# Performance work log

Hardware: AMD Instinct MI355X
Metric: run time of the kernel (lower is better)

Reference implementation:

```python
import jax, jax.numpy as jnp
import numpy as np

# --- config (matches init_kwargs) ---
B, L = 16, 1024            # batch, max_seq_len
S = L - 1                  # effective sequence length
D = 768                    # attention_dim
H = 8                      # n_heads
DH = D // 3 * 2            # per-head Q/K/V out dim = 512
HID = 256                  # hidden_dim (EntireEmbedding output)
FF = 3072                  # ffnn_dim
N_A = 10000                # n_assessments = offsets[0]
N_CATE, N_CONT = 4, 6
EPS = 1e-5


def setup_inputs() -> dict:
    key = jax.random.key(0)
    ks = jax.random.split(key, 24)
    f = lambda k, shp, s=0.02: (jax.random.normal(k, shp, dtype=jnp.float32) * s)
    inp = {
        "cate_x": jax.random.randint(ks[0], (B, L, N_CATE), 0, N_A),
        "cont_x": jax.random.normal(ks[1], (B, L, N_CONT), dtype=jnp.float32),
        "mask": jax.random.randint(ks[2], (B, L), 0, 2),
        "targets": jax.random.randint(ks[3], (B, L), 0, 2),
        # embeddings (padding_idx=0 rows zeroed)
        "M_emb": f(ks[4], ((N_A + 1) * 2 - 1, D)).at[0].set(0.0),
        "E_emb": f(ks[5], (N_A + 1, D)).at[0].set(0.0),
        "pos_emb": f(ks[6], (S, D)),
        # EntireEmbedding stand-in: cate embedding + linear over cont feats -> HID
        "cate_emb": f(ks[7], (N_A + 1, HID)).at[0].set(0.0),
        "cont_W": f(ks[8], (N_CONT, HID)),
        "cont_b": jnp.zeros((HID,), jnp.float32),
        # per-head Q/K/V, stacked over head axis
        "WQ": f(ks[9], (H, D, DH)),
        "bQ": jnp.zeros((H, DH), jnp.float32),
        "WK": f(ks[10], (H, D + HID, DH)),
        "bK": jnp.zeros((H, DH), jnp.float32),
        "WV": f(ks[11], (H, D + HID, DH)),
        "bV": jnp.zeros((H, DH), jnp.float32),
        "W0": f(ks[12], (H * DH, D)),
        "ln_g": jnp.ones((D,), jnp.float32),
        "ln_b": jnp.zeros((D,), jnp.float32),
        "ffn_W1": f(ks[13], (D, FF)),
        "ffn_b1": jnp.zeros((FF,), jnp.float32),
        "ffn_W2": f(ks[14], (FF, D)),
        "ffn_b2": jnp.zeros((D,), jnp.float32),
        # FinalConnecting stand-in: Linear(D, 1)
        "fin_W": f(ks[15], (D, 1)),
        "fin_b": jnp.zeros((1,), jnp.float32),
    }
    return inp


def reference(cate_x, cont_x, mask, targets, M_emb, E_emb, pos_emb, cate_emb,
              cont_W, cont_b, WQ, bQ, WK, bK, WV, bV, W0, ln_g, ln_b,
              ffn_W1, ffn_b1, ffn_W2, ffn_b2, fin_W, fin_b):
    # additive mask, faithful to the original (triu over [B,S]!)
    new_mask = jnp.triu(jnp.ones((B, S), jnp.float32), k=-1) * 100000.0 - 100000.0

    assessments = cate_x[:, :-1, 0]                 # [B,S]
    interactions = targets[:, :-1]
    y = assessments + interactions * N_A            # interaction ids
    next_assessments = cate_x[:, 1:, 0]

    M_hat = M_emb[y] + pos_emb[None]                # [B,S,D]
    comb = cate_emb[cate_x[..., 0]] + cont_x @ cont_W + cont_b   # [B,L,HID]
    E_hat = jnp.concatenate([E_emb[next_assessments], comb[:, 1:, :]], axis=-1)  # [B,S,D+HID]

    # all heads at once (faithful per-head Q/K/V linears, stacked)
    Q = jnp.einsum('bsd,hde->hbse', M_hat, WQ) + bQ[:, None, None, :]
    K = jnp.einsum('bsd,hde->hbse', E_hat, WK) + bK[:, None, None, :]
    V = jnp.einsum('bsd,hde->hbse', E_hat, WV) + bV[:, None, None, :]

    score = jnp.einsum('hbqe,hbke->hbqk', Q, K) / jnp.sqrt(jnp.asarray(DH, Q.dtype))
    score = score + new_mask[None, :, None, :]      # broadcast over query axis
    attn = jax.nn.softmax(score, axis=-1)
    Z = jnp.einsum('hbqk,hbke->hbqe', attn, V)      # [H,B,S,DH]
    Zc = jnp.transpose(Z, (1, 2, 0, 3)).reshape(B, S, H * DH)  # head-major concat

    z = Zc @ W0                                     # [B,S,D]
    fz = jax.nn.relu(z @ ffn_W1 + ffn_b1) @ ffn_W2 + ffn_b2  # dropout off (eval)
    h = z + fz
    mu = jnp.mean(h, axis=-1, keepdims=True)
    var = jnp.mean((h - mu) ** 2, axis=-1, keepdims=True)
    zn = (h - mu) / jnp.sqrt(var + EPS) * ln_g + ln_b

    out = (zn @ fin_W + fin_b)[..., 0]              # [B,S]
    return out
```

## Files before the change

kernel.cpp:

```cpp
#include <hip/hip_runtime.h>
#include <hip/hip_bf16.h>

constexpr int B_   = 16;
constexpr int L_   = 1024;
constexpr int S_   = 1023;
constexpr int D_   = 768;
constexpr int H_   = 8;
constexpr int DH_  = 512;
constexpr int HID_ = 256;
constexpr int FF_  = 3072;
constexpr int NA_  = 10000;
constexpr int NCATE_ = 4;
constexpr int NCONT_ = 6;
constexpr float EPS_ = 1e-5f;
constexpr long BSR_ = (long)B_ * S_;
constexpr int SLD_ = 1024;

constexpr long COMB_SZ = BSR_ * HID_;
constexpr long IDX_PAD = 49152;
constexpr long QKV_SZ  = BSR_ * DH_;
constexpr long SC_SZ   = (long)B_ * S_ * SLD_;
constexpr long ZO_SZ   = BSR_ * D_;
constexpr size_t WS_NEED_BYTES =
    (size_t)(COMB_SZ + IDX_PAD + 3 * QKV_SZ + SC_SZ + ZO_SZ) * 4;

__device__ __forceinline__ float blk_reduce_sum(float v, float* sm) {
#pragma unroll
    for (int off = 32; off > 0; off >>= 1) v += __shfl_down(v, off, 64);
    const int lane = threadIdx.x & 63, wv = threadIdx.x >> 6;
    if (lane == 0) sm[wv] = v;
    __syncthreads();
    float t = (threadIdx.x < 4) ? sm[threadIdx.x] : 0.f;
    t += __shfl_down(t, 2, 64);
    t += __shfl_down(t, 1, 64);
    if (threadIdx.x == 0) sm[4] = t;
    __syncthreads();
    float r = sm[4];
    __syncthreads();
    return r;
}

__device__ __forceinline__ float blk_reduce_max(float v, float* sm) {
#pragma unroll
    for (int off = 32; off > 0; off >>= 1) v = fmaxf(v, __shfl_down(v, off, 64));
    const int lane = threadIdx.x & 63, wv = threadIdx.x >> 6;
    if (lane == 0) sm[wv] = v;
    __syncthreads();
    float t = (threadIdx.x < 4) ? sm[threadIdx.x] : -3.4e38f;
    t = fmaxf(t, __shfl_down(t, 2, 64));
    t = fmaxf(t, __shfl_down(t, 1, 64));
    if (threadIdx.x == 0) sm[4] = t;
    __syncthreads();
    float r = sm[4];
    __syncthreads();
    return r;
}

__global__ __launch_bounds__(256) void sentinel_k(float* __restrict__ out, int n)
{
    const int i = blockIdx.x * 256 + threadIdx.x;
    if (i < n) out[i] = 1e30f;
}

__global__ __launch_bounds__(256) void prep_k(
    const int* __restrict__ cate_x, const float* __restrict__ cont_x,
    const int* __restrict__ targets,
    const float* __restrict__ cate_emb, const float* __restrict__ cont_W,
    const float* __restrict__ cont_b,
    int* __restrict__ yArr, int* __restrict__ nxArr, int* __restrict__ sArr,
    float* __restrict__ comb)
{
    const int row = blockIdx.x;
    const int b = row / S_;
    const int s = row - b * S_;
    const int nx = cate_x[((long)b * L_ + s + 1) * NCATE_];
    if (threadIdx.x == 0) {
        yArr[row]  = cate_x[((long)b * L_ + s) * NCATE_] + targets[(long)b * L_ + s] * NA_;
        nxArr[row] = nx;
        sArr[row]  = s;
    }
    const float* cx = cont_x + ((long)b * L_ + s + 1) * NCONT_;
    float cv[NCONT_];
#pragma unroll
    for (int i = 0; i < NCONT_; ++i) cv[i] = cx[i];
    const int j = threadIdx.x;
    float acc = cont_b[j];
#pragma unroll
    for (int i = 0; i < NCONT_; ++i) acc = fmaf(cv[i], cont_W[i * HID_ + j], acc);
    comb[(long)row * HID_ + j] = cate_emb[(long)nx * HID_ + j] + acc;
}

template<int AMODE, bool TB, bool BIAS, bool RELU, bool ADDC, bool ACCUM>
__global__ __launch_bounds__(256) void sgemm_k(
    const float* __restrict__ A, const float* __restrict__ A2,
    const int* __restrict__ rIdx, const int* __restrict__ rS,
    const float* __restrict__ Bm,
    const float* __restrict__ bias, const float* __restrict__ Cadd,
    float* __restrict__ C,
    int M, int N, int Kd, int lda, int ldb, int ldc,
    long sA, long sB, long sC, float alpha)
{
    constexpr int BM = 128, BN = 128, BK = 16;
    __shared__ float As[BK][BM];
    __shared__ float Bs[BK][BN];

    const int tid = threadIdx.x;
    const int tx = tid & 15;
    const int ty = tid >> 4;
    const int rowBase = blockIdx.y * BM;
    const int colBase = blockIdx.x * BN;
    const int bz = blockIdx.z;
    if constexpr (AMODE == 0) A += (long)bz * sA;
    Bm += (long)bz * sB;
    C += (long)bz * sC;
    if constexpr (ADDC) Cadd += (long)bz * sC;

    float acc[8][8];
#pragma unroll
    for (int i = 0; i < 8; ++i)
#pragma unroll
        for (int j = 0; j < 8; ++j) acc[i][j] = 0.f;

    for (int k0 = 0; k0 < Kd; k0 += BK) {
#pragma unroll
        for (int u = 0; u < 2; ++u) {
            const int f = tid + u * 256;
            const int r = f >> 2;
            const int k4 = (f & 3) * 4;
            const int gk = k0 + k4;
            float v0 = 0.f, v1 = 0.f, v2 = 0.f, v3 = 0.f;
            const int gr = rowBase + r;
            if (gr < M) {
                if constexpr (AMODE == 0) {
                    const float* p = A + (long)gr * lda + gk;
                    if (gk + 3 < Kd) {
                        float4 v = *(const float4*)p;
                        v0 = v.x; v1 = v.y; v2 = v.z; v3 = v.w;
                    } else {
                        if (gk + 0 < Kd) v0 = p[0];
                        if (gk + 1 < Kd) v1 = p[1];
                        if (gk + 2 < Kd) v2 = p[2];
                        if (gk + 3 < Kd) v3 = p[3];
                    }
                } else if constexpr (AMODE == 1) {
                    const int y = rIdx[gr];
                    const int s = rS[gr];
                    const float4 a = *(const float4*)(A  + (long)y * D_ + gk);
                    const float4 p = *(const float4*)(A2 + (long)s * D_ + gk);
                    v0 = a.x + p.x; v1 = a.y + p.y; v2 = a.z + p.z; v3 = a.w + p.w;
                } else {
                    if (gk < D_) {
                        const int nx = rIdx[gr];
                        const float4 a = *(const float4*)(A + (long)nx * D_ + gk);
                        v0 = a.x; v1 = a.y; v2 = a.z; v3 = a.w;
                    } else {
                        const float4 a = *(const float4*)(A2 + (long)gr * HID_ + (gk - D_));
                        v0 = a.x; v1 = a.y; v2 = a.z; v3 = a.w;
                    }
                }
            }
            As[k4 + 0][r] = v0; As[k4 + 1][r] = v1;
            As[k4 + 2][r] = v2; As[k4 + 3][r] = v3;
        }
        if constexpr (!TB) {
#pragma unroll
            for (int u = 0; u < 2; ++u) {
                const int f = tid + u * 256;
                const int kk = f >> 5;
                const int n4 = (f & 31) * 4;
                float v0 = 0.f, v1 = 0.f, v2 = 0.f, v3 = 0.f;
                const int gk = k0 + kk;
                const int gc = colBase + n4;
                if (gk < Kd) {
                    const float* p = Bm + (long)gk * ldb + gc;
                    if (gc + 3 < N) {
                        float4 v = *(const float4*)p;
                        v0 = v.x; v1 = v.y; v2 = v.z; v3 = v.w;
                    } else {
                        if (gc + 0 < N) v0 = p[0];
                        if (gc + 1 < N) v1 = p[1];
                        if (gc + 2 < N) v2 = p[2];
                        if (gc + 3 < N) v3 = p[3];
                    }
                }
                Bs[kk][n4 + 0] = v0; Bs[kk][n4 + 1] = v1;
                Bs[kk][n4 + 2] = v2; Bs[kk][n4 + 3] = v3;
            }
        } else {
#pragma unroll
            for (int u = 0; u < 2; ++u) {
                const int f = tid + u * 256;
                const int n = f >> 2;
                const int k4 = (f & 3) * 4;
                float v0 = 0.f, v1 = 0.f, v2 = 0.f, v3 = 0.f;
                const int gn = colBase + n;
                if (gn < N) {
                    const float* p = Bm + (long)gn * ldb + k0 + k4;
                    if (k0 + k4 + 3 < Kd) {
                        float4 v = *(const float4*)p;
                        v0 = v.x; v1 = v.y; v2 = v.z; v3 = v.w;
                    } else {
                        if (k0 + k4 + 0 < Kd) v0 = p[0];
                        if (k0 + k4 + 1 < Kd) v1 = p[1];
                        if (k0 + k4 + 2 < Kd) v2 = p[2];
                        if (k0 + k4 + 3 < Kd) v3 = p[3];
                    }
                }
                Bs[k4 + 0][n] = v0; Bs[k4 + 1][n] = v1;
                Bs[k4 + 2][n] = v2; Bs[k4 + 3][n] = v3;
            }
        }
        __syncthreads();

#pragma unroll
        for (int kk = 0; kk < BK; ++kk) {
            float a[8], b[8];
            *(float4*)&a[0] = *(const float4*)&As[kk][ty * 8];
            *(float4*)&a[4] = *(const float4*)&As[kk][ty * 8 + 4];
            *(float4*)&b[0] = *(const float4*)&Bs[kk][tx * 8];
            *(float4*)&b[4] = *(const float4*)&Bs[kk][tx * 8 + 4];
#pragma unroll
            for (int i = 0; i < 8; ++i)
#pragma unroll
                for (int j = 0; j < 8; ++j)
                    acc[i][j] = fmaf(a[i], b[j], acc[i][j]);
        }
        __syncthreads();
    }

#pragma unroll
    for (int i = 0; i < 8; ++i) {
        const int r = rowBase + ty * 8 + i;
        if (r >= M) continue;
#pragma unroll
        for (int j = 0; j < 8; ++j) {
            const int c = colBase + tx * 8 + j;
            if (c >= N) continue;
            float v = acc[i][j] * alpha;
            if constexpr (BIAS) v += bias[c];
            if constexpr (ADDC) v += Cadd[(long)r * ldc + c];
            if constexpr (RELU) v = fmaxf(v, 0.f);
            const long idx = (long)r * ldc + c;
            if constexpr (ACCUM) C[idx] += v; else C[idx] = v;
        }
    }
}

__global__ __launch_bounds__(256) void softmax_k(float* __restrict__ Sc)
{
    const int row = blockIdx.x;
    const int b = row / S_;
    float* s = Sc + (long)row * SLD_;
    __shared__ float buf[S_];
    __shared__ float sm[5];
    const int klo = b - 1;

    float m = -3.4e38f;
    for (int k = threadIdx.x; k < S_; k += 256) {
        float v = s[k];
        if (k < klo) v -= 1e5f;
        buf[k] = v;
        m = fmaxf(m, v);
    }
    m = blk_reduce_max(m, sm);
    float sum = 0.f;
    for (int k = threadIdx.x; k < S_; k += 256) {
        const float e = __expf(buf[k] - m);
        buf[k] = e;
        sum += e;
    }
    sum = blk_reduce_sum(sum, sm);
    const float inv = 1.0f / sum;
    for (int k = threadIdx.x; k < S_; k += 256) s[k] = buf[k] * inv;
}

__global__ __launch_bounds__(256) void final_k(
    const float* __restrict__ h, const float* __restrict__ g,
    const float* __restrict__ bt, const float* __restrict__ fw,
    const float* __restrict__ fb, float* __restrict__ out)
{
    const int row = blockIdx.x;
    const float* hr = h + (long)row * D_;
    __shared__ float sm[5];

    float lsum = 0.f;
    for (int d = threadIdx.x; d < D_; d += 256) lsum += hr[d];
    const float mu = blk_reduce_sum(lsum, sm) * (1.0f / D_);

    float lvar = 0.f;
    for (int d = threadIdx.x; d < D_; d += 256) {
        const float t = hr[d] - mu;
        lvar = fmaf(t, t, lvar);
    }
    const float var = blk_reduce_sum(lvar, sm) * (1.0f / D_);
    const float rstd = 1.0f / sqrtf(var + EPS_);

    float ldot = 0.f;
    for (int d = threadIdx.x; d < D_; d += 256) {
        const float zn = (hr[d] - mu) * rstd * g[d] + bt[d];
        ldot = fmaf(zn, fw[d], ldot);
    }
    const float dot = blk_reduce_sum(ldot, sm);
    if (threadIdx.x == 0) out[row] = dot + fb[0];
}

static inline dim3 gemm_grid(int M, int N, int batch) {
    return dim3((N + 127) / 128, (M + 127) / 128, batch);
}

extern "C" void kernel_launch(void* const* d_in, const int* in_sizes, int n_in,
                              void* d_out, int out_size, void* d_ws, size_t ws_size,
                              hipStream_t stream)
{
    float* out = (float*)d_out;

    if (ws_size < WS_NEED_BYTES) {
        sentinel_k<<<(out_size + 255) / 256, 256, 0, stream>>>(out, out_size);
        return;
    }

    const int*   cate_x   = (const int*)  d_in[0];
    const float* cont_x   = (const float*)d_in[1];
    const int*   targets  = (const int*)  d_in[3];
    const float* M_emb    = (const float*)d_in[4];
    const float* E_emb    = (const float*)d_in[5];
    const float* pos_emb  = (const float*)d_in[6];
    const float* cate_emb = (const float*)d_in[7];
    const float* cont_W   = (const float*)d_in[8];
    const float* cont_b   = (const float*)d_in[9];
    const float* WQ = (const float*)d_in[10];
    const float* bQ = (const float*)d_in[11];
    const float* WK = (const float*)d_in[12];
    const float* bK = (const float*)d_in[13];
    const float* WV = (const float*)d_in[14];
    const float* bV = (const float*)d_in[15];
    const float* W0 = (const float*)d_in[16];
    const float* ln_g = (const float*)d_in[17];
    const float* ln_b = (const float*)d_in[18];
    const float* W1 = (const float*)d_in[19];
    const float* b1 = (const float*)d_in[20];
    const float* W2 = (const float*)d_in[21];
    const float* b2 = (const float*)d_in[22];
    const float* fw = (const float*)d_in[23];
    const float* fb = (const float*)d_in[24];
    float* ws  = (float*)d_ws;

    float* comb  = ws;
    int*   yArr  = (int*)(ws + COMB_SZ);
    int*   nxArr = yArr + BSR_;
    int*   sArr  = nxArr + BSR_;
    float* Qh = ws + COMB_SZ + IDX_PAD;
    float* Kh = Qh + QKV_SZ;
    float* Vh = Kh + QKV_SZ;
    float* Sc = Vh + QKV_SZ;
    float* Zo = Sc + SC_SZ;
    float* Zh   = Qh;
    float* Hid  = Qh;
    float* Hbuf = Sc;

    prep_k<<<(int)BSR_, 256, 0, stream>>>(cate_x, cont_x, targets, cate_emb,
                                          cont_W, cont_b, yArr, nxArr, sArr, comb);

    const float inv_sqrt_dh = 0.044194173824159216f;

    for (int h = 0; h < H_; ++h) {
        sgemm_k<1, false, true, false, false, false><<<gemm_grid((int)BSR_, DH_, 1), 256, 0, stream>>>(
            M_emb, pos_emb, yArr, sArr,
            WQ + (long)h * D_ * DH_, bQ + (long)h * DH_, nullptr, Qh,
            (int)BSR_, DH_, D_, D_, DH_, DH_, 0, 0, 0, 1.0f);
        sgemm_k<2, false, true, false, false, false><<<gemm_grid((int)BSR_, DH_, 1), 256, 0, stream>>>(
            E_emb, comb, nxArr, nullptr,
            WK + (long)h * (D_ + HID_) * DH_, bK + (long)h * DH_, nullptr, Kh,
            (int)BSR_, DH_, D_ + HID_, 0, DH_, DH_, 0, 0, 0, 1.0f);
        sgemm_k<2, false, true, false, false, false><<<gemm_grid((int)BSR_, DH_, 1), 256, 0, stream>>>(
            E_emb, comb, nxArr, nullptr,
            WV + (long)h * (D_ + HID_) * DH_, bV + (long)h * DH_, nullptr, Vh,
            (int)BSR_, DH_, D_ + HID_, 0, DH_, DH_, 0, 0, 0, 1.0f);
        sgemm_k<0, true, false, false, false, false><<<gemm_grid(S_, S_, B_), 256, 0, stream>>>(
            Qh, nullptr, nullptr, nullptr,
            Kh, nullptr, nullptr, Sc,
            S_, S_, DH_, DH_, DH_, SLD_,
            (long)S_ * DH_, (long)S_ * DH_, (long)S_ * SLD_, inv_sqrt_dh);
        softmax_k<<<(int)BSR_, 256, 0, stream>>>(Sc);
        sgemm_k<0, false, false, false, false, false><<<gemm_grid(S_, DH_, B_), 256, 0, stream>>>(
            Sc, nullptr, nullptr, nullptr,
            Vh, nullptr, nullptr, Zh,
            S_, DH_, S_, SLD_, DH_, DH_,
            (long)S_ * SLD_, (long)S_ * DH_, (long)S_ * DH_, 1.0f);
        if (h == 0)
            sgemm_k<0, false, false, false, false, false><<<gemm_grid((int)BSR_, D_, 1), 256, 0, stream>>>(
                Zh, nullptr, nullptr, nullptr,
                W0 + (long)h * DH_ * D_, nullptr, nullptr, Zo,
                (int)BSR_, D_, DH_, DH_, D_, D_, 0, 0, 0, 1.0f);
        else
            sgemm_k<0, false, false, false, false, true><<<gemm_grid((int)BSR_, D_, 1), 256, 0, stream>>>(
                Zh, nullptr, nullptr, nullptr,
                W0 + (long)h * DH_ * D_, nullptr, nullptr, Zo,
                (int)BSR_, D_, DH_, DH_, D_, D_, 0, 0, 0, 1.0f);
    }

    for (int c = 0; c < 4; ++c) {
        const int f0 = c * 768;
        sgemm_k<0, false, true, true, false, false><<<gemm_grid((int)BSR_, 768, 1), 256, 0, stream>>>(
            Zo, nullptr, nullptr, nullptr,
            W1 + f0, b1 + f0, nullptr, Hid,
            (int)BSR_, 768, D_, D_, FF_, 768, 0, 0, 0, 1.0f);
        if (c == 0)
            sgemm_k<0, false, true, false, true, false><<<gemm_grid((int)BSR_, D_, 1), 256, 0, stream>>>(
                Hid, nullptr, nullptr, nullptr,
                W2 + (long)f0 * D_, b2, Zo, Hbuf,
                (int)BSR_, D_, 768, 768, D_, D_, 0, 0, 0, 1.0f);
        else
            sgemm_k<0, false, false, false, false, true><<<gemm_grid((int)BSR_, D_, 1), 256, 0, stream>>>(
                Hid, nullptr, nullptr, nullptr,
                W2 + (long)f0 * D_, nullptr, nullptr, Hbuf,
                (int)BSR_, D_, 768, 768, D_, D_, 0, 0, 0, 1.0f);
    }

    final_k<<<(int)BSR_, 256, 0, stream>>>(Hbuf, ln_g, ln_b, fw, fb, out);

    (void)in_sizes; (void)n_in;
}
```

Before: 13.02 ms.

## Parametrize SGEMM tile size, fuse K/V projections, and interleave thread tile mapping

Makes the SGEMM tile size a template parameter, using 64x64 tiles with 4x4 per-thread micro-tiles for most GEMMs and keeping 128x128 tiles for the QK^T score GEMM. The K and V projections now run in a single launch, with column blocks past DH routed to the V weights, bias and output. Each thread's elements are now strided by 64 in shared memory and the output, instead of sitting in one contiguous block of 8. The aim is more blocks in flight on the mid-size GEMMs and fewer launches and LDS conflicts. The cost is lower arithmetic intensity per thread with 4x4 micro-tiles.

```diff
diff --git a/kernel.cpp b/kernel.cpp
--- a/kernel.cpp
+++ b/kernel.cpp
@@ -90,40 +90,53 @@
     comb[(long)row * HID_ + j] = cate_emb[(long)nx * HID_ + j] + acc;
 }
 
-template<int AMODE, bool TB, bool BIAS, bool RELU, bool ADDC, bool ACCUM>
+template<int TSZ, int AMODE, bool TB, bool BIAS, bool RELU, bool ADDC, bool ACCUM, bool KVF>
 __global__ __launch_bounds__(256) void sgemm_k(
     const float* __restrict__ A, const float* __restrict__ A2,
     const int* __restrict__ rIdx, const int* __restrict__ rS,
-    const float* __restrict__ Bm,
-    const float* __restrict__ bias, const float* __restrict__ Cadd,
-    float* __restrict__ C,
+    const float* __restrict__ Bm, const float* __restrict__ Bm2,
+    const float* __restrict__ bias, const float* __restrict__ bias2,
+    const float* __restrict__ Cadd, float* __restrict__ C, float* __restrict__ C2,
     int M, int N, int Kd, int lda, int ldb, int ldc,
     long sA, long sB, long sC, float alpha)
 {
-    constexpr int BM = 128, BN = 128, BK = 16;
-    __shared__ float As[BK][BM];
-    __shared__ float Bs[BK][BN];
+    constexpr int BK = 16;
+    constexpr int TM = TSZ / 16;
+    constexpr int NL = TSZ / 64;
+    constexpr int NF4M = TSZ / 4 - 1;
+    constexpr int SHB  = (TSZ == 128) ? 5 : 4;
+    __shared__ float As[BK][TSZ];
+    __shared__ float Bs[BK][TSZ];
 
     const int tid = threadIdx.x;
     const int tx = tid & 15;
     const int ty = tid >> 4;
-    const int rowBase = blockIdx.y * BM;
-    const int colBase = blockIdx.x * BN;
+    const int rowBase = blockIdx.y * TSZ;
+    int colBase = blockIdx.x * TSZ;
     const int bz = blockIdx.z;
+
+    if constexpr (KVF) {
+        if (colBase >= DH_) {
+            Bm = Bm2;
+            if constexpr (BIAS) bias = bias2;
+            C = C2;
+            colBase -= DH_;
+        }
+    }
     if constexpr (AMODE == 0) A += (long)bz * sA;
     Bm += (long)bz * sB;
     C += (long)bz * sC;
     if constexpr (ADDC) Cadd += (long)bz * sC;
 
-    float acc[8][8];
-#pragma unroll
-    for (int i = 0; i < 8; ++i)
-#pragma unroll
-        for (int j = 0; j < 8; ++j) acc[i][j] = 0.f;
+    float acc[TM][TM];
+#pragma unroll
+    for (int i = 0; i < TM; ++i)
+#pragma unroll
+        for (int j = 0; j < TM; ++j) acc[i][j] = 0.f;
 
     for (int k0 = 0; k0 < Kd; k0 += BK) {
 #pragma unroll
-        for (int u = 0; u < 2; ++u) {
+        for (int u = 0; u < NL; ++u) {
             const int f = tid + u * 256;
             const int r = f >> 2;
             const int k4 = (f & 3) * 4;
@@ -140,7 +153,6 @@
                         if (gk + 0 < Kd) v0 = p[0];
                         if (gk + 1 < Kd) v1 = p[1];
                         if (gk + 2 < Kd) v2 = p[2];
-                        if (gk + 3 < Kd) v3 = p[3];
                     }
                 } else if constexpr (AMODE == 1) {
                     const int y = rIdx[gr];
@@ -164,13 +176,13 @@
         }
         if constexpr (!TB) {
 #pragma unroll
-            for (int u = 0; u < 2; ++u) {
+            for (int u = 0; u < NL; ++u) {
                 const int f = tid + u * 256;
-                const int kk = f >> 5;
-                const int n4 = (f & 31) * 4;
-                float v0 = 0.f, v1 = 0.f, v2 = 0.f, v3 = 0.f;
+                const int kk = f >> SHB;
+                const int n4 = (f & NF4M) * 4;
                 const int gk = k0 + kk;
                 const int gc = colBase + n4;
+                float v0 = 0.f, v1 = 0.f, v2 = 0.f, v3 = 0.f;
                 if (gk < Kd) {
                     const float* p = Bm + (long)gk * ldb + gc;
                     if (gc + 3 < N) {
@@ -188,7 +200,7 @@
             }
         } else {
 #pragma unroll
-            for (int u = 0; u < 2; ++u) {
+            for (int u = 0; u < NL; ++u) {
                 const int f = tid + u * 256;
                 const int n = f >> 2;
                 const int k4 = (f & 3) * 4;
@@ -214,27 +226,28 @@
 
 #pragma unroll
         for (int kk = 0; kk < BK; ++kk) {
-            float a[8], b[8];
-            *(float4*)&a[0] = *(const float4*)&As[kk][ty * 8];
-            *(float4*)&a[4] = *(const float4*)&As[kk][ty * 8 + 4];
-            *(float4*)&b[0] = *(const float4*)&Bs[kk][tx * 8];
-            *(float4*)&b[4] = *(const float4*)&Bs[kk][tx * 8 + 4];
-#pragma unroll
-            for (int i = 0; i < 8; ++i)
-#pragma unroll
-                for (int j = 0; j < 8; ++j)
+            float a[TM], b[TM];
+#pragma unroll
+            for (int ih = 0; ih < TM / 4; ++ih) {
+                *(float4*)&a[ih * 4] = *(const float4*)&As[kk][ih * 64 + ty * 4];
+                *(float4*)&b[ih * 4] = *(const float4*)&Bs[kk][ih * 64 + tx * 4];
+            }
+#pragma unroll
+            for (int i = 0; i < TM; ++i)
+#pragma unroll
+                for (int j = 0; j < TM; ++j)
                     acc[i][j] = fmaf(a[i], b[j], acc[i][j]);
         }
         __syncthreads();
     }
 
 #pragma unroll
-    for (int i = 0; i < 8; ++i) {
-        const int r = rowBase + ty * 8 + i;
+    for (int i = 0; i < TM; ++i) {
+        const int r = rowBase + (i >> 2) * 64 + ty * 4 + (i & 3);
         if (r >= M) continue;
 #pragma unroll
-        for (int j = 0; j < 8; ++j) {
-            const int c = colBase + tx * 8 + j;
+        for (int j = 0; j < TM; ++j) {
+            const int c = colBase + (j >> 2) * 64 + tx * 4 + (j & 3);
             if (c >= N) continue;
             float v = acc[i][j] * alpha;
             if constexpr (BIAS) v += bias[c];
@@ -304,8 +317,8 @@
     if (threadIdx.x == 0) out[row] = dot + fb[0];
 }
 
-static inline dim3 gemm_grid(int M, int N, int batch) {
-    return dim3((N + 127) / 128, (M + 127) / 128, batch);
+static inline dim3 ggrid(int M, int N, int batch, int tsz) {
+    return dim3((N + tsz - 1) / tsz, (M + tsz - 1) / tsz, batch);
 }
 
 extern "C" void kernel_launch(void* const* d_in, const int* in_sizes, int n_in,
@@ -313,7 +326,6 @@
                               hipStream_t stream)
 {
     float* out = (float*)d_out;
-
     if (ws_size < WS_NEED_BYTES) {
         sentinel_k<<<(out_size + 255) / 256, 256, 0, stream>>>(out, out_size);
         return;
@@ -364,56 +376,71 @@
     const float inv_sqrt_dh = 0.044194173824159216f;
 
     for (int h = 0; h < H_; ++h) {
-        sgemm_k<1, false, true, false, false, false><<<gemm_grid((int)BSR_, DH_, 1), 256, 0, stream>>>(
+        sgemm_k<64, 1, false, true, false, false, false, false>
+            <<<ggrid((int)BSR_, DH_, 1, 64), 256, 0, stream>>>(
             M_emb, pos_emb, yArr, sArr,
-            WQ + (long)h * D_ * DH_, bQ + (long)h * DH_, nullptr, Qh,
+            WQ + (long)h * D_ * DH_, nullptr, bQ + (long)h * DH_, nullptr,
+            nullptr, Qh, nullptr,
             (int)BSR_, DH_, D_, D_, DH_, DH_, 0, 0, 0, 1.0f);
-        sgemm_k<2, false, true, false, false, false><<<gemm_grid((int)BSR_, DH_, 1), 256, 0, stream>>>(
+        sgemm_k<64, 2, false, true, false, false, false, true>
+            <<<ggrid((int)BSR_, 2 * DH_, 1, 64), 256, 0, stream>>>(
             E_emb, comb, nxArr, nullptr,
-            WK + (long)h * (D_ + HID_) * DH_, bK + (long)h * DH_, nullptr, Kh,
-            (int)BSR_, DH_, D_ + HID_, 0, DH_, DH_, 0, 0, 0, 1.0f);
-        sgemm_k<2, false, true, false, false, false><<<gemm_grid((int)BSR_, DH_, 1), 256, 0, stream>>>(
-            E_emb, comb, nxArr, nullptr,
-            WV + (long)h * (D_ + HID_) * DH_, bV + (long)h * DH_, nullptr, Vh,
-            (int)BSR_, DH_, D_ + HID_, 0, DH_, DH_, 0, 0, 0, 1.0f);
-        sgemm_k<0, true, false, false, false, false><<<gemm_grid(S_, S_, B_), 256, 0, stream>>>(
+            WK + (long)h * (D_ + HID_) * DH_, WV + (long)h * (D_ + HID_) * DH_,
+            bK + (long)h * DH_, bV + (long)h * DH_,
+            nullptr, Kh, Vh,
+            (int)BSR_, 2 * DH_, D_ + HID_, 0, DH_, DH_, 0, 0, 0, 1.0f);
+        sgemm_k<128, 0, true, false, false, false, false, false>
+            <<<ggrid(S_, S_, B_, 128), 256, 0, stream>>>(
             Qh, nullptr, nullptr, nullptr,
-            Kh, nullptr, nullptr, Sc,
+            Kh, nullptr, nullptr, nullptr,
+            nullptr, Sc, nullptr,
             S_, S_, DH_, DH_, DH_, SLD_,
             (long)S_ * DH_, (long)S_ * DH_, (long)S_ * SLD_, inv_sqrt_dh);
         softmax_k<<<(int)BSR_, 256, 0, stream>>>(Sc);
-        sgemm_k<0, false, false, false, false, false><<<gemm_grid(S_, DH_, B_), 256, 0, stream>>>(
+        sgemm_k<64, 0, false, false, false, false, false, false>
+            <<<ggrid(S_, DH_, B_, 64), 256, 0, stream>>>(
             Sc, nullptr, nullptr, nullptr,
-            Vh, nullptr, nullptr, Zh,
+            Vh, nullptr, nullptr, nullptr,
+            nullptr, Zh, nullptr,
             S_, DH_, S_, SLD_, DH_, DH_,
             (long)S_ * SLD_, (long)S_ * DH_, (long)S_ * DH_, 1.0f);
         if (h == 0)
-            sgemm_k<0, false, false, false, false, false><<<gemm_grid((int)BSR_, D_, 1), 256, 0, stream>>>(
+            sgemm_k<64, 0, false, false, false, false, false, false>
+                <<<ggrid((int)BSR_, D_, 1, 64), 256, 0, stream>>>(
                 Zh, nullptr, nullptr, nullptr,
-                W0 + (long)h * DH_ * D_, nullptr, nullptr, Zo,
+                W0 + (long)h * DH_ * D_, nullptr, nullptr, nullptr,
+                nullptr, Zo, nullptr,
                 (int)BSR_, D_, DH_, DH_, D_, D_, 0, 0, 0, 1.0f);
         else
-            sgemm_k<0, false, false, false, false, true><<<gemm_grid((int)BSR_, D_, 1), 256, 0, stream>>>(
+            sgemm_k<64, 0, false, false, false, false, true, false>
+                <<<ggrid((int)BSR_, D_, 1, 64), 256, 0, stream>>>(
                 Zh, nullptr, nullptr, nullptr,
-                W0 + (long)h * DH_ * D_, nullptr, nullptr, Zo,
+                W0 + (long)h * DH_ * D_, nullptr, nullptr, nullptr,
+                nullptr, Zo, nullptr,
                 (int)BSR_, D_, DH_, DH_, D_, D_, 0, 0, 0, 1.0f);
     }
 
     for (int c = 0; c < 4; ++c) {
         const int f0 = c * 768;
-        sgemm_k<0, false, true, true, false, false><<<gemm_grid((int)BSR_, 768, 1), 256, 0, stream>>>(
+        sgemm_k<64, 0, false, true, true, false, false, false>
+            <<<ggrid((int)BSR_, 768, 1, 64), 256, 0, stream>>>(
             Zo, nullptr, nullptr, nullptr,
-            W1 + f0, b1 + f0, nullptr, Hid,
+            W1 + f0, nullptr, b1 + f0, nullptr,
+            nullptr, Hid, nullptr,
             (int)BSR_, 768, D_, D_, FF_, 768, 0, 0, 0, 1.0f);
         if (c == 0)
-            sgemm_k<0, false, true, false, true, false><<<gemm_grid((int)BSR_, D_, 1), 256, 0, stream>>>(
+            sgemm_k<64, 0, false, true, false, true, false, false>
+                <<<ggrid((int)BSR_, D_, 1, 64), 256, 0, stream>>>(
                 Hid, nullptr, nullptr, nullptr,
-                W2 + (long)f0 * D_, b2, Zo, Hbuf,
+                W2 + (long)f0 * D_, nullptr, b2, nullptr,
+                Zo, Hbuf, nullptr,
                 (int)BSR_, D_, 768, 768, D_, D_, 0, 0, 0, 1.0f);
         else
-            sgemm_k<0, false, false, false, false, true><<<gemm_grid((int)BSR_, D_, 1), 256, 0, stream>>>(
+            sgemm_k<64, 0, false, false, false, false, true, false>
+                <<<ggrid((int)BSR_, D_, 1, 64), 256, 0, stream>>>(
                 Hid, nullptr, nullptr, nullptr,
-                W2 + (long)f0 * D_, nullptr, nullptr, Hbuf,
+                W2 + (long)f0 * D_, nullptr, nullptr, nullptr,
+                nullptr, Hbuf, nullptr,
                 (int)BSR_, D_, 768, 768, D_, D_, 0, 0, 0, 1.0f);
     }
 
```

Result: no change. 12.93 ms (-0.7%).
